# Kernel optimization log

Measured on AMD Instinct MI355X. Metric: run time of the kernel, lower is better.

## Reference

```python
import jax, jax.numpy as jnp
import numpy as np

NUM_BINS_X = 128; NUM_BINS_Y = 128
XL, XH, YL, YH = 0.0, 1000.0, 0.0, 1000.0
NUM_NETS = 100000
NUM_NODES = 200000
NUM_MOVABLE = 180000
NUM_PINS = 400000
UNIT_H_CAP = 1.5
UNIT_V_CAP = 1.4
MAX_RATE = 2.0
MIN_RATE = 1.0 / MAX_RATE
BIN_SX = (XH - XL) / NUM_BINS_X
BIN_SY = (YH - YL) / NUM_BINS_Y


def setup_inputs() -> dict:
    key = jax.random.key(0)
    k1, k2, k3, k4, k5, k6, k7, k8 = jax.random.split(key, 8)
    pos = jnp.concatenate([
        jax.random.uniform(k1, (NUM_NODES,), jnp.float32, XL, XH - 8.0),
        jax.random.uniform(k2, (NUM_NODES,), jnp.float32, YL, YH - 8.0)])
    pin_pos = jnp.concatenate([
        jax.random.uniform(k3, (NUM_PINS,), jnp.float32, XL, XH),
        jax.random.uniform(k4, (NUM_PINS,), jnp.float32, YL, YH)])
    node_size_x = jax.random.uniform(k5, (NUM_NODES,), jnp.float32, 1.0, 8.0)
    node_size_y = jax.random.uniform(k6, (NUM_NODES,), jnp.float32, 1.0, 8.0)
    # 4 pins per net (uniform ragged layout); flat_netpin is a permutation of pins
    netpin_start = jnp.arange(NUM_NETS + 1, dtype=jnp.int32) * (NUM_PINS // NUM_NETS)
    flat_netpin = jax.random.permutation(k7, NUM_PINS).astype(jnp.int32)
    net_weights = jax.random.uniform(k8, (NUM_NETS,), jnp.float32, 0.5, 1.5)
    return dict(pos=pos, pin_pos=pin_pos, node_size_x=node_size_x,
                node_size_y=node_size_y, net_weights=net_weights,
                netpin_start=netpin_start, flat_netpin=flat_netpin)


def _bin_edges(lo, size, n):
    l = lo + jnp.arange(n, dtype=jnp.float32) * size
    return l, l + size


def _overlap(lo_e, hi_e, lo, hi):
    # per-interval overlap of [lo, hi] with each bin [lo_e, hi_e]; >=0
    return jnp.clip(jnp.minimum(hi_e[None, :], hi[:, None]) -
                    jnp.maximum(lo_e[None, :], lo[:, None]), 0.0, None)


def reference(pos, pin_pos, node_size_x, node_size_y, net_weights,
              netpin_start, flat_netpin):
    # ---- phase 1: per-net bbox (ragged gather) + RUDY demand binning ----
    lengths = netpin_start[1:] - netpin_start[:-1]                      # [N]
    net_ids = jnp.repeat(jnp.arange(NUM_NETS, dtype=jnp.int32), lengths,
                         total_repeat_length=NUM_PINS)                  # [P]
    px = pin_pos[flat_netpin]
    py = pin_pos[flat_netpin + NUM_PINS]
    x_min = jax.ops.segment_min(px, net_ids, num_segments=NUM_NETS)
    x_max = jax.ops.segment_max(px, net_ids, num_segments=NUM_NETS)
    y_min = jax.ops.segment_min(py, net_ids, num_segments=NUM_NETS)
    y_max = jax.ops.segment_max(py, net_ids, num_segments=NUM_NETS)

    bxl, bxr = _bin_edges(XL, BIN_SX, NUM_BINS_X)
    byl, byr = _bin_edges(YL, BIN_SY, NUM_BINS_Y)
    ox = _overlap(bxl, bxr, x_min, x_max)                               # [N, BX]
    oy = _overlap(byl, byr, y_min, y_max)                               # [N, BY]
    dx = x_max - x_min
    dy = y_max - y_min
    # horizontal demand per bin = wt * overlap / (y_max - y_min); vertical analog
    cx = jnp.where(dy > 0, net_weights / jnp.where(dy > 0, dy, 1.0), 0.0)
    cy = jnp.where(dx > 0, net_weights / jnp.where(dx > 0, dx, 1.0), 0.0)
    map_x = jnp.einsum('nx,ny->xy', ox * cx[:, None], oy)               # [BX, BY]
    map_y = jnp.einsum('nx,ny->xy', ox * cy[:, None], oy)

    bin_area = BIN_SX * BIN_SY
    ux = map_x / (bin_area * UNIT_H_CAP)
    uy = map_y / (bin_area * UNIT_V_CAP)
    util = jnp.clip(jnp.maximum(ux, uy), MIN_RATE, MAX_RATE)            # [BX, BY]

    # ---- phase 2: per movable node, overlap-weighted utilization read-back ----
    nx = pos[:NUM_MOVABLE]
    ny = pos[NUM_NODES:NUM_NODES + NUM_MOVABLE]
    sx = node_size_x[:NUM_MOVABLE]
    sy = node_size_y[:NUM_MOVABLE]
    oxn = _overlap(bxl, bxr, nx, nx + sx)                               # [M, BX]
    oyn = _overlap(byl, byr, ny, ny + sy)                               # [M, BY]
    tmp = jnp.einsum('mx,xy->my', oxn, util)                            # [M, BY]
    instance_route_area = jnp.sum(tmp * oyn, axis=1)                    # [M]
    return instance_route_area
```

## Files before the change

### kernel.cpp

```cpp
#include <hip/hip_runtime.h>

constexpr int   NB         = 128;
constexpr int   NCELL      = NB * NB;
constexpr int   NFL        = 2 * NCELL;
constexpr float S          = 7.8125f;
constexpr int   NUM_NETS   = 100000;
constexpr int   NUM_NODES  = 200000;
constexpr int   NUM_MOVABLE= 180000;
constexpr int   NUM_PINS   = 400000;
constexpr float UNIT_H_CAP = 1.5f;
constexpr float UNIT_V_CAP = 1.4f;

#define TPB    1024
#define NDB    256
#define NCHUNK 8

__device__ __forceinline__ float edgef(int t) { return (float)t * S; }

__device__ __forceinline__ int bin_of(float v) {
    int t = (int)floorf(v / S);
    while (edgef(t + 1) <= v) ++t;
    while (edgef(t)     >  v) --t;
    return t;
}

__device__ __forceinline__ float phi(int t, float lo, float hi) {
    return fminf(fmaxf(edgef(t), lo), hi);
}

__global__ __launch_bounds__(TPB) void net_diff_kernel(
    const float* __restrict__ pin_pos,
    const float* __restrict__ net_weights,
    const int*   __restrict__ nps,
    const int*   __restrict__ fnp,
    float* __restrict__ P) {
    extern __shared__ float Dl[];
    const int tid = threadIdx.x;

    float4* D4 = (float4*)Dl;
    for (int i = tid; i < NFL / 4; i += TPB) D4[i] = make_float4(0, 0, 0, 0);
    __syncthreads();

    const int per = (NUM_NETS + gridDim.x - 1) / gridDim.x;
    const int n0  = blockIdx.x * per;
    const int n1  = min(n0 + per, NUM_NETS);
    const int l   = tid & 3;
    const int g   = tid >> 2;
    constexpr int GP = TPB / 4;

    for (int n = n0 + g; n < n1; n += GP) {
        int s = nps[n], e = nps[n + 1];
        bool ok = (e > s);
        float xmin, xmax, ymin, ymax;
        if (ok && (e - s == 4)) {
            int pin = fnp[s + l];
            float xv = pin_pos[pin];
            float yv = pin_pos[pin + NUM_PINS];
            xmin = xv; xmax = xv; ymin = yv; ymax = yv;
        } else {
            xmin = 1e30f; xmax = -1e30f; ymin = 1e30f; ymax = -1e30f;
            if (ok && l == 0) {
                for (int p = s; p < e; ++p) {
                    int pin = fnp[p];
                    float px = pin_pos[pin];
                    float py = pin_pos[pin + NUM_PINS];
                    xmin = fminf(xmin, px); xmax = fmaxf(xmax, px);
                    ymin = fminf(ymin, py); ymax = fmaxf(ymax, py);
                }
            }
        }
        xmin = fminf(xmin, __shfl_xor(xmin, 1));
        xmin = fminf(xmin, __shfl_xor(xmin, 2));
        xmax = fmaxf(xmax, __shfl_xor(xmax, 1));
        xmax = fmaxf(xmax, __shfl_xor(xmax, 2));
        ymin = fminf(ymin, __shfl_xor(ymin, 1));
        ymin = fminf(ymin, __shfl_xor(ymin, 2));
        ymax = fmaxf(ymax, __shfl_xor(ymax, 1));
        ymax = fmaxf(ymax, __shfl_xor(ymax, 2));
        if (!ok) continue;

        float w  = net_weights[n];
        float dx = xmax - xmin, dy = ymax - ymin;
        float cx = (dy > 0.f) ? w / dy : 0.f;
        float cy = (dx > 0.f) ? w / dx : 0.f;
        if (cx == 0.f && cy == 0.f) continue;

        int ax = bin_of(xmin), bx = bin_of(xmax);
        int row; bool has;
        if      (l == 0) { row = ax;     has = true; }
        else if (l == 1) { row = ax + 1; has = true; }
        else if (l == 2) { row = bx;     has = (bx > ax + 1); }
        else             { row = bx + 1; has = (bx > ax); }
        if (!has || row >= NB) continue;
        float fi = phi(row + 1, xmin, xmax) - 2.f * phi(row, xmin, xmax)
                 + phi(row - 1, xmin, xmax);
        if (fi == 0.f) continue;

        int ay = bin_of(ymin), by = bin_of(ymax);
        #pragma unroll
        for (int j = 0; j < 4; ++j) {
            int col; bool hj;
            if      (j == 0) { col = ay;     hj = true; }
            else if (j == 1) { col = ay + 1; hj = true; }
            else if (j == 2) { col = by;     hj = (by > ay + 1); }
            else             { col = by + 1; hj = (by > ay); }
            if (!hj || col >= NB) continue;
            float fj = phi(col + 1, ymin, ymax) - 2.f * phi(col, ymin, ymax)
                     + phi(col - 1, ymin, ymax);
            float t = fi * fj;
            if (t == 0.f) continue;
            int cell = row * NB + col;
            if (cx != 0.f) atomicAdd(&Dl[cell],         cx * t);
            if (cy != 0.f) atomicAdd(&Dl[NCELL + cell], cy * t);
        }
    }
    __syncthreads();

    float4* Pb = (float4*)(P + (size_t)blockIdx.x * NFL);
    for (int i = tid; i < NFL / 4; i += TPB) Pb[i] = D4[i];
}

__global__ __launch_bounds__(256) void reduce_kernel(
    const float4* __restrict__ P,
    float4* __restrict__ Rc,
    int B) {
    constexpr int NF4 = NFL / 4;
    int g = blockIdx.y * blockDim.x + threadIdx.x;
    int chunk = blockIdx.x;
    float4 a0 = {0,0,0,0}, a1 = {0,0,0,0}, a2 = {0,0,0,0}, a3 = {0,0,0,0};
    int b = chunk;
    for (; b + 3 * NCHUNK < B; b += 4 * NCHUNK) {
        float4 v0 = P[(size_t)(b             ) * NF4 + g];
        float4 v1 = P[(size_t)(b +     NCHUNK) * NF4 + g];
        float4 v2 = P[(size_t)(b + 2 * NCHUNK) * NF4 + g];
        float4 v3 = P[(size_t)(b + 3 * NCHUNK) * NF4 + g];
        a0.x += v0.x; a0.y += v0.y; a0.z += v0.z; a0.w += v0.w;
        a1.x += v1.x; a1.y += v1.y; a1.z += v1.z; a1.w += v1.w;
        a2.x += v2.x; a2.y += v2.y; a2.z += v2.z; a2.w += v2.w;
        a3.x += v3.x; a3.y += v3.y; a3.z += v3.z; a3.w += v3.w;
    }
    for (; b < B; b += NCHUNK) {
        float4 v = P[(size_t)b * NF4 + g];
        a0.x += v.x; a0.y += v.y; a0.z += v.z; a0.w += v.w;
    }
    float4 r;
    r.x = (a0.x + a1.x) + (a2.x + a3.x);
    r.y = (a0.y + a1.y) + (a2.y + a3.y);
    r.z = (a0.z + a1.z) + (a2.z + a3.z);
    r.w = (a0.w + a1.w) + (a2.w + a3.w);
    Rc[(size_t)chunk * NF4 + g] = r;
}

__global__ __launch_bounds__(NB) void scan_x_kernel(
    const float* __restrict__ Rc,
    float2* __restrict__ Xp) {
    __shared__ float2 sm[NB];
    int col = blockIdx.x;
    int t = threadIdx.x;
    int idx = t * NB + col;
    float2 v = make_float2(0.f, 0.f);
    #pragma unroll
    for (int c = 0; c < NCHUNK; ++c) {
        v.x += Rc[(size_t)c * NFL + idx];
        v.y += Rc[(size_t)c * NFL + NCELL + idx];
    }
    sm[t] = v;
    __syncthreads();
    #pragma unroll
    for (int off = 1; off < NB; off <<= 1) {
        float2 cur = sm[t];
        float2 add = (t >= off) ? sm[t - off] : make_float2(0.f, 0.f);
        __syncthreads();
        cur.x += add.x; cur.y += add.y;
        sm[t] = cur;
        __syncthreads();
    }
    Xp[idx] = sm[t];
}

__global__ __launch_bounds__(NB) void scan_y_kernel(
    const float2* __restrict__ Xp,
    float* __restrict__ util) {
    __shared__ float2 sm[NB];
    int row = blockIdx.x;
    int t = threadIdx.x;
    sm[t] = Xp[row * NB + t];
    __syncthreads();
    #pragma unroll
    for (int off = 1; off < NB; off <<= 1) {
        float2 cur = sm[t];
        float2 add = (t >= off) ? sm[t - off] : make_float2(0.f, 0.f);
        __syncthreads();
        cur.x += add.x; cur.y += add.y;
        sm[t] = cur;
        __syncthreads();
    }
    constexpr float invx = 1.f / (S * S * UNIT_H_CAP);
    constexpr float invy = 1.f / (S * S * UNIT_V_CAP);
    float2 r = sm[t];
    float u = fmaxf(r.x * invx, r.y * invy);
    util[row * NB + t] = fminf(fmaxf(u, 0.5f), 2.0f);
}

__global__ __launch_bounds__(256) void node_kernel(
    const float* __restrict__ pos,
    const float* __restrict__ nsx,
    const float* __restrict__ nsy,
    const float* __restrict__ util,
    float* __restrict__ out) {
    int m = blockIdx.x * blockDim.x + threadIdx.x;
    if (m >= NUM_MOVABLE) return;
    float x  = pos[m];
    float y  = pos[NUM_NODES + m];
    float xh = x + nsx[m];
    float yh = y + nsy[m];
    int ax = max(0,      (int)floorf(x  / S) - 1);
    int bx = min(NB - 1, (int)floorf(xh / S) + 1);
    int ay = max(0,      (int)floorf(y  / S) - 1);
    int by = min(NB - 1, (int)floorf(yh / S) + 1);
    float acc = 0.f;
    for (int i = ax; i <= bx; ++i) {
        float ov = fminf(edgef(i + 1), xh) - fmaxf(edgef(i), x);
        if (ov <= 0.f) continue;
        float inner = 0.f;
        for (int j = ay; j <= by; ++j) {
            float ovy = fminf(edgef(j + 1), yh) - fmaxf(edgef(j), y);
            if (ovy > 0.f) inner += ovy * util[i * NB + j];
        }
        acc += ov * inner;
    }
    out[m] = acc;
}

extern "C" void kernel_launch(void* const* d_in, const int* in_sizes, int n_in,
                              void* d_out, int out_size, void* d_ws, size_t ws_size,
                              hipStream_t stream) {
    const float* pos      = (const float*)d_in[0];
    const float* pin_pos  = (const float*)d_in[1];
    const float* nsx      = (const float*)d_in[2];
    const float* nsy      = (const float*)d_in[3];
    const float* nw       = (const float*)d_in[4];
    const int*   npstart  = (const int*)d_in[5];
    const int*   fnp      = (const int*)d_in[6];
    float*       out      = (float*)d_out;

    float* w    = (float*)d_ws;
    float* Rc   = w;                           w += NCHUNK * NFL;
    float* Xp   = w;                           w += NFL;
    float* util = w;                           w += NCELL;
    float* P    = w;

    size_t fixed = (size_t)(w - (float*)d_ws) * sizeof(float);
    int B = NDB;
    if (ws_size > fixed) {
        size_t fit = (ws_size - fixed) / ((size_t)NFL * sizeof(float));
        if ((size_t)B > fit) B = (int)fit;
    } else {
        B = 1;
    }
    if (B < 1) B = 1;

    (void)hipFuncSetAttribute((const void*)net_diff_kernel,
                              hipFuncAttributeMaxDynamicSharedMemorySize,
                              NFL * (int)sizeof(float));

    net_diff_kernel<<<B, TPB, NFL * sizeof(float), stream>>>(
        pin_pos, nw, npstart, fnp, P);
    {
        dim3 g(NCHUNK, NFL / 4 / 256);
        reduce_kernel<<<g, 256, 0, stream>>>(
            (const float4*)P, (float4*)Rc, B);
    }
    scan_x_kernel<<<NB, NB, 0, stream>>>(Rc, (float2*)Xp);
    scan_y_kernel<<<NB, NB, 0, stream>>>((const float2*)Xp, util);
    node_kernel<<<(NUM_MOVABLE + 255) / 256, 256, 0, stream>>>(
        pos, nsx, nsy, util, out);
}
```

Measured before the change: 115.0 us.

## Split RUDY maps across block pairs and fuse the two prefix scans

Each net-binning block now accumulates only one demand map, horizontal or vertical, chosen by block parity. This halves the per-block LDS histogram and halves the partial-map traffic written to and read back from global memory. The cost is that every net's bounding box is gathered and computed twice, once per map type. The separate x and y scan kernels are replaced by one single-block kernel that runs serial column and row scans in padded LDS. That removes a launch and the intermediate buffer, but leaves only 128 threads doing the serial work.

Measured after the change: 124.6 us. 1.08x slower.

```diff
diff --git a/kernel.cpp b/kernel.cpp
--- a/kernel.cpp
+++ b/kernel.cpp
@@ -2,7 +2,6 @@
 
 constexpr int   NB         = 128;
 constexpr int   NCELL      = NB * NB;
-constexpr int   NFL        = 2 * NCELL;
 constexpr float S          = 7.8125f;
 constexpr int   NUM_NETS   = 100000;
 constexpr int   NUM_NODES  = 200000;
@@ -13,7 +12,9 @@
 
 #define TPB    1024
 #define NDB    256
+#define NET_LDS_BYTES (96*1024)
 #define NCHUNK 8
+#define PAD    129
 
 __device__ __forceinline__ float edgef(int t) { return (float)t * S; }
 
@@ -38,11 +39,14 @@
     const int tid = threadIdx.x;
 
     float4* D4 = (float4*)Dl;
-    for (int i = tid; i < NFL / 4; i += TPB) D4[i] = make_float4(0, 0, 0, 0);
-    __syncthreads();
-
-    const int per = (NUM_NETS + gridDim.x - 1) / gridDim.x;
-    const int n0  = blockIdx.x * per;
+    for (int i = tid; i < NCELL / 4; i += TPB) D4[i] = make_float4(0, 0, 0, 0);
+    __syncthreads();
+
+    const int nchunks = (int)(gridDim.x >> 1);
+    const int chunk   = (int)(blockIdx.x >> 1);
+    const int type    = (int)(blockIdx.x & 1);
+    const int per = (NUM_NETS + nchunks - 1) / nchunks;
+    const int n0  = chunk * per;
     const int n1  = min(n0 + per, NUM_NETS);
     const int l   = tid & 3;
     const int g   = tid >> 2;
@@ -81,9 +85,9 @@
 
         float w  = net_weights[n];
         float dx = xmax - xmin, dy = ymax - ymin;
-        float cx = (dy > 0.f) ? w / dy : 0.f;
-        float cy = (dx > 0.f) ? w / dx : 0.f;
-        if (cx == 0.f && cy == 0.f) continue;
+        float c  = (type == 0) ? ((dy > 0.f) ? w / dy : 0.f)
+                               : ((dx > 0.f) ? w / dx : 0.f);
+        if (c == 0.f) continue;
 
         int ax = bin_of(xmin), bx = bin_of(xmax);
         int row; bool has;
@@ -109,38 +113,36 @@
                      + phi(col - 1, ymin, ymax);
             float t = fi * fj;
             if (t == 0.f) continue;
-            int cell = row * NB + col;
-            if (cx != 0.f) atomicAdd(&Dl[cell],         cx * t);
-            if (cy != 0.f) atomicAdd(&Dl[NCELL + cell], cy * t);
-        }
-    }
-    __syncthreads();
-
-    float4* Pb = (float4*)(P + (size_t)blockIdx.x * NFL);
-    for (int i = tid; i < NFL / 4; i += TPB) Pb[i] = D4[i];
+            atomicAdd(&Dl[row * NB + col], c * t);
+        }
+    }
+    __syncthreads();
+
+    float4* Pb = (float4*)(P + (size_t)blockIdx.x * NCELL);
+    for (int i = tid; i < NCELL / 4; i += TPB) Pb[i] = D4[i];
 }
 
 __global__ __launch_bounds__(256) void reduce_kernel(
     const float4* __restrict__ P,
     float4* __restrict__ Rc,
     int B) {
-    constexpr int NF4 = NFL / 4;
-    int g = blockIdx.y * blockDim.x + threadIdx.x;
+    constexpr int NQ = NCELL / 4;
+    int g = blockIdx.y * 256 + threadIdx.x;
     int chunk = blockIdx.x;
     float4 a0 = {0,0,0,0}, a1 = {0,0,0,0}, a2 = {0,0,0,0}, a3 = {0,0,0,0};
     int b = chunk;
     for (; b + 3 * NCHUNK < B; b += 4 * NCHUNK) {
-        float4 v0 = P[(size_t)(b             ) * NF4 + g];
-        float4 v1 = P[(size_t)(b +     NCHUNK) * NF4 + g];
-        float4 v2 = P[(size_t)(b + 2 * NCHUNK) * NF4 + g];
-        float4 v3 = P[(size_t)(b + 3 * NCHUNK) * NF4 + g];
+        float4 v0 = P[(size_t)(b             ) * NQ + g];
+        float4 v1 = P[(size_t)(b +     NCHUNK) * NQ + g];
+        float4 v2 = P[(size_t)(b + 2 * NCHUNK) * NQ + g];
+        float4 v3 = P[(size_t)(b + 3 * NCHUNK) * NQ + g];
         a0.x += v0.x; a0.y += v0.y; a0.z += v0.z; a0.w += v0.w;
         a1.x += v1.x; a1.y += v1.y; a1.z += v1.z; a1.w += v1.w;
         a2.x += v2.x; a2.y += v2.y; a2.z += v2.z; a2.w += v2.w;
         a3.x += v3.x; a3.y += v3.y; a3.z += v3.z; a3.w += v3.w;
     }
     for (; b < B; b += NCHUNK) {
-        float4 v = P[(size_t)b * NF4 + g];
+        float4 v = P[(size_t)b * NQ + g];
         a0.x += v.x; a0.y += v.y; a0.z += v.z; a0.w += v.w;
     }
     float4 r;
@@ -148,58 +150,48 @@
     r.y = (a0.y + a1.y) + (a2.y + a3.y);
     r.z = (a0.z + a1.z) + (a2.z + a3.z);
     r.w = (a0.w + a1.w) + (a2.w + a3.w);
-    Rc[(size_t)chunk * NF4 + g] = r;
-}
-
-__global__ __launch_bounds__(NB) void scan_x_kernel(
+    Rc[(size_t)chunk * NQ + g] = r;
+}
+
+__global__ __launch_bounds__(1024) void scanxy_kernel(
     const float* __restrict__ Rc,
-    float2* __restrict__ Xp) {
-    __shared__ float2 sm[NB];
-    int col = blockIdx.x;
-    int t = threadIdx.x;
-    int idx = t * NB + col;
-    float2 v = make_float2(0.f, 0.f);
-    #pragma unroll
-    for (int c = 0; c < NCHUNK; ++c) {
-        v.x += Rc[(size_t)c * NFL + idx];
-        v.y += Rc[(size_t)c * NFL + NCELL + idx];
-    }
-    sm[t] = v;
-    __syncthreads();
-    #pragma unroll
-    for (int off = 1; off < NB; off <<= 1) {
-        float2 cur = sm[t];
-        float2 add = (t >= off) ? sm[t - off] : make_float2(0.f, 0.f);
-        __syncthreads();
-        cur.x += add.x; cur.y += add.y;
-        sm[t] = cur;
-        __syncthreads();
-    }
-    Xp[idx] = sm[t];
-}
-
-__global__ __launch_bounds__(NB) void scan_y_kernel(
-    const float2* __restrict__ Xp,
     float* __restrict__ util) {
-    __shared__ float2 sm[NB];
-    int row = blockIdx.x;
-    int t = threadIdx.x;
-    sm[t] = Xp[row * NB + t];
-    __syncthreads();
-    #pragma unroll
-    for (int off = 1; off < NB; off <<= 1) {
-        float2 cur = sm[t];
-        float2 add = (t >= off) ? sm[t - off] : make_float2(0.f, 0.f);
-        __syncthreads();
-        cur.x += add.x; cur.y += add.y;
-        sm[t] = cur;
-        __syncthreads();
-    }
-    constexpr float invx = 1.f / (S * S * UNIT_H_CAP);
-    constexpr float invy = 1.f / (S * S * UNIT_V_CAP);
-    float2 r = sm[t];
-    float u = fmaxf(r.x * invx, r.y * invy);
-    util[row * NB + t] = fminf(fmaxf(u, 0.5f), 2.0f);
+    extern __shared__ float2 M[];
+    int tid = threadIdx.x;
+    for (int cell = tid; cell < NCELL; cell += 1024) {
+        int r = cell >> 7, c = cell & (NB - 1);
+        float vx = Rc[0 * NCELL + cell] + Rc[2 * NCELL + cell]
+                 + Rc[4 * NCELL + cell] + Rc[6 * NCELL + cell];
+        float vy = Rc[1 * NCELL + cell] + Rc[3 * NCELL + cell]
+                 + Rc[5 * NCELL + cell] + Rc[7 * NCELL + cell];
+        M[r * PAD + c] = make_float2(vx, vy);
+    }
+    __syncthreads();
+    if (tid < NB) {
+        int col = tid;
+        float2 acc = M[col];
+        for (int r = 1; r < NB; ++r) {
+            float2 v = M[r * PAD + col];
+            acc.x += v.x; acc.y += v.y;
+            M[r * PAD + col] = acc;
+        }
+    }
+    __syncthreads();
+    if (tid < NB) {
+        int row = tid;
+        constexpr float invx = 1.f / (S * S * UNIT_H_CAP);
+        constexpr float invy = 1.f / (S * S * UNIT_V_CAP);
+        float2 acc = make_float2(0.f, 0.f);
+        for (int c = 0; c < NB; ++c) {
+            float2 v = M[row * PAD + c];
+            acc.x += v.x; acc.y += v.y;
+            float u = fmaxf(acc.x * invx, acc.y * invy);
+            M[row * PAD + c].x = fminf(fmaxf(u, 0.5f), 2.0f);
+        }
+    }
+    __syncthreads();
+    for (int cell = tid; cell < NCELL; cell += 1024)
+        util[cell] = M[(cell >> 7) * PAD + (cell & (NB - 1))].x;
 }
 
 __global__ __launch_bounds__(256) void node_kernel(
@@ -245,34 +237,37 @@
     float*       out      = (float*)d_out;
 
     float* w    = (float*)d_ws;
-    float* Rc   = w;                           w += NCHUNK * NFL;
-    float* Xp   = w;                           w += NFL;
+    float* Rc   = w;                           w += NCHUNK * NCELL;
     float* util = w;                           w += NCELL;
     float* P    = w;
 
     size_t fixed = (size_t)(w - (float*)d_ws) * sizeof(float);
     int B = NDB;
     if (ws_size > fixed) {
-        size_t fit = (ws_size - fixed) / ((size_t)NFL * sizeof(float));
+        size_t fit = (ws_size - fixed) / ((size_t)NCELL * sizeof(float));
         if ((size_t)B > fit) B = (int)fit;
     } else {
-        B = 1;
-    }
-    if (B < 1) B = 1;
+        B = 2;
+    }
+    B &= ~1;
+    if (B < 2) B = 2;
 
     (void)hipFuncSetAttribute((const void*)net_diff_kernel,
                               hipFuncAttributeMaxDynamicSharedMemorySize,
-                              NFL * (int)sizeof(float));
-
-    net_diff_kernel<<<B, TPB, NFL * sizeof(float), stream>>>(
+                              NET_LDS_BYTES);
+    (void)hipFuncSetAttribute((const void*)scanxy_kernel,
+                              hipFuncAttributeMaxDynamicSharedMemorySize,
+                              NB * PAD * (int)sizeof(float2));
+
+    net_diff_kernel<<<B, TPB, NET_LDS_BYTES, stream>>>(
         pin_pos, nw, npstart, fnp, P);
     {
-        dim3 g(NCHUNK, NFL / 4 / 256);
+        dim3 g(NCHUNK, NCELL / 4 / 256);
         reduce_kernel<<<g, 256, 0, stream>>>(
             (const float4*)P, (float4*)Rc, B);
     }
-    scan_x_kernel<<<NB, NB, 0, stream>>>(Rc, (float2*)Xp);
-    scan_y_kernel<<<NB, NB, 0, stream>>>((const float2*)Xp, util);
+    scanxy_kernel<<<1, 1024, NB * PAD * (int)sizeof(float2), stream>>>(
+        Rc, util);
     node_kernel<<<(NUM_MOVABLE + 255) / 256, 256, 0, stream>>>(
         pos, nsx, nsy, util, out);
 }
```

## Fuse 2D prefix scans into one LDS kernel and process two nets per iteration

Applied to the files above, without the earlier changes.

Replaces the separate column and row scan kernels, and the global intermediate buffer between them, with a single 1024-thread block. That block does both prefix passes in padded LDS using segmented scans. Separately, the net binning loop now handles two nets per iteration, issuing both nets' gathers before either scatter so memory latency overlaps. The single-block scan cuts a launch and a global round trip, but runs on one CU with 16-step serial segments. The two-net loop raises register pressure.

New measurement: 126.1 us. 1.1x slower.

```diff
diff --git a/kernel.cpp b/kernel.cpp
--- a/kernel.cpp
+++ b/kernel.cpp
@@ -15,6 +15,10 @@
 #define NDB    256
 #define NCHUNK 8
 
+#define PADM2  129
+#define SEG    8
+#define SEGR   16
+
 __device__ __forceinline__ float edgef(int t) { return (float)t * S; }
 
 __device__ __forceinline__ int bin_of(float v) {
@@ -26,6 +30,56 @@
 
 __device__ __forceinline__ float phi(int t, float lo, float hi) {
     return fminf(fmaxf(edgef(t), lo), hi);
+}
+
+__device__ __forceinline__ void grp_reduce(float& xmin, float& xmax,
+                                           float& ymin, float& ymax) {
+    xmin = fminf(xmin, __shfl_xor(xmin, 1));
+    xmin = fminf(xmin, __shfl_xor(xmin, 2));
+    xmax = fmaxf(xmax, __shfl_xor(xmax, 1));
+    xmax = fmaxf(xmax, __shfl_xor(xmax, 2));
+    ymin = fminf(ymin, __shfl_xor(ymin, 1));
+    ymin = fminf(ymin, __shfl_xor(ymin, 2));
+    ymax = fmaxf(ymax, __shfl_xor(ymax, 1));
+    ymax = fmaxf(ymax, __shfl_xor(ymax, 2));
+}
+
+__device__ __forceinline__ void scatter_net(
+    float xmin, float xmax, float ymin, float ymax, float w,
+    int l, float* __restrict__ Dl) {
+    float dx = xmax - xmin, dy = ymax - ymin;
+    float cx = (dy > 0.f) ? w / dy : 0.f;
+    float cy = (dx > 0.f) ? w / dx : 0.f;
+    if (cx == 0.f && cy == 0.f) return;
+
+    int ax = bin_of(xmin), bx = bin_of(xmax);
+    int row; bool has;
+    if      (l == 0) { row = ax;     has = true; }
+    else if (l == 1) { row = ax + 1; has = true; }
+    else if (l == 2) { row = bx;     has = (bx > ax + 1); }
+    else             { row = bx + 1; has = (bx > ax); }
+    if (!has || row >= NB) return;
+    float fi = phi(row + 1, xmin, xmax) - 2.f * phi(row, xmin, xmax)
+             + phi(row - 1, xmin, xmax);
+    if (fi == 0.f) return;
+
+    int ay = bin_of(ymin), by = bin_of(ymax);
+    #pragma unroll
+    for (int j = 0; j < 4; ++j) {
+        int col; bool hj;
+        if      (j == 0) { col = ay;     hj = true; }
+        else if (j == 1) { col = ay + 1; hj = true; }
+        else if (j == 2) { col = by;     hj = (by > ay + 1); }
+        else             { col = by + 1; hj = (by > ay); }
+        if (!hj || col >= NB) continue;
+        float fj = phi(col + 1, ymin, ymax) - 2.f * phi(col, ymin, ymax)
+                 + phi(col - 1, ymin, ymax);
+        float t = fi * fj;
+        if (t == 0.f) continue;
+        int cell = row * NB + col;
+        if (cx != 0.f) atomicAdd(&Dl[cell],         cx * t);
+        if (cy != 0.f) atomicAdd(&Dl[NCELL + cell], cy * t);
+    }
 }
 
 __global__ __launch_bounds__(TPB) void net_diff_kernel(
@@ -48,70 +102,59 @@
     const int g   = tid >> 2;
     constexpr int GP = TPB / 4;
 
-    for (int n = n0 + g; n < n1; n += GP) {
-        int s = nps[n], e = nps[n + 1];
-        bool ok = (e > s);
-        float xmin, xmax, ymin, ymax;
-        if (ok && (e - s == 4)) {
-            int pin = fnp[s + l];
-            float xv = pin_pos[pin];
-            float yv = pin_pos[pin + NUM_PINS];
-            xmin = xv; xmax = xv; ymin = yv; ymax = yv;
-        } else {
-            xmin = 1e30f; xmax = -1e30f; ymin = 1e30f; ymax = -1e30f;
-            if (ok && l == 0) {
-                for (int p = s; p < e; ++p) {
-                    int pin = fnp[p];
-                    float px = pin_pos[pin];
-                    float py = pin_pos[pin + NUM_PINS];
-                    xmin = fminf(xmin, px); xmax = fmaxf(xmax, px);
-                    ymin = fminf(ymin, py); ymax = fmaxf(ymax, py);
+    for (int nA = n0 + g; nA < n1; nA += 2 * GP) {
+        const int nB = nA + GP;
+        const bool hasB = (nB < n1);
+
+        int sA = nps[nA], eA = nps[nA + 1];
+        int sB = 0, eB = 0;
+        if (hasB) { sB = nps[nB]; eB = nps[nB + 1]; }
+        const bool okA = (eA > sA), okB = hasB && (eB > sB);
+        const bool fA = okA && (eA - sA == 4);
+        const bool fB = okB && (eB - sB == 4);
+        int pinA = fA ? fnp[sA + l] : 0;
+        int pinB = fB ? fnp[sB + l] : 0;
+        float xvA = 0.f, yvA = 0.f, xvB = 0.f, yvB = 0.f;
+        if (fA) { xvA = pin_pos[pinA]; yvA = pin_pos[pinA + NUM_PINS]; }
+        if (fB) { xvB = pin_pos[pinB]; yvB = pin_pos[pinB + NUM_PINS]; }
+        float wA = okA ? net_weights[nA] : 0.f;
+        float wB = okB ? net_weights[nB] : 0.f;
+
+        {
+            float xmin, xmax, ymin, ymax;
+            if (fA) { xmin = xvA; xmax = xvA; ymin = yvA; ymax = yvA; }
+            else {
+                xmin = 1e30f; xmax = -1e30f; ymin = 1e30f; ymax = -1e30f;
+                if (okA && l == 0) {
+                    for (int p = sA; p < eA; ++p) {
+                        int pin = fnp[p];
+                        float px = pin_pos[pin];
+                        float py = pin_pos[pin + NUM_PINS];
+                        xmin = fminf(xmin, px); xmax = fmaxf(xmax, px);
+                        ymin = fminf(ymin, py); ymax = fmaxf(ymax, py);
+                    }
                 }
             }
-        }
-        xmin = fminf(xmin, __shfl_xor(xmin, 1));
-        xmin = fminf(xmin, __shfl_xor(xmin, 2));
-        xmax = fmaxf(xmax, __shfl_xor(xmax, 1));
-        xmax = fmaxf(xmax, __shfl_xor(xmax, 2));
-        ymin = fminf(ymin, __shfl_xor(ymin, 1));
-        ymin = fminf(ymin, __shfl_xor(ymin, 2));
-        ymax = fmaxf(ymax, __shfl_xor(ymax, 1));
-        ymax = fmaxf(ymax, __shfl_xor(ymax, 2));
-        if (!ok) continue;
-
-        float w  = net_weights[n];
-        float dx = xmax - xmin, dy = ymax - ymin;
-        float cx = (dy > 0.f) ? w / dy : 0.f;
-        float cy = (dx > 0.f) ? w / dx : 0.f;
-        if (cx == 0.f && cy == 0.f) continue;
-
-        int ax = bin_of(xmin), bx = bin_of(xmax);
-        int row; bool has;
-        if      (l == 0) { row = ax;     has = true; }
-        else if (l == 1) { row = ax + 1; has = true; }
-        else if (l == 2) { row = bx;     has = (bx > ax + 1); }
-        else             { row = bx + 1; has = (bx > ax); }
-        if (!has || row >= NB) continue;
-        float fi = phi(row + 1, xmin, xmax) - 2.f * phi(row, xmin, xmax)
-                 + phi(row - 1, xmin, xmax);
-        if (fi == 0.f) continue;
-
-        int ay = bin_of(ymin), by = bin_of(ymax);
-        #pragma unroll
-        for (int j = 0; j < 4; ++j) {
-            int col; bool hj;
-            if      (j == 0) { col = ay;     hj = true; }
-            else if (j == 1) { col = ay + 1; hj = true; }
-            else if (j == 2) { col = by;     hj = (by > ay + 1); }
-            else             { col = by + 1; hj = (by > ay); }
-            if (!hj || col >= NB) continue;
-            float fj = phi(col + 1, ymin, ymax) - 2.f * phi(col, ymin, ymax)
-                     + phi(col - 1, ymin, ymax);
-            float t = fi * fj;
-            if (t == 0.f) continue;
-            int cell = row * NB + col;
-            if (cx != 0.f) atomicAdd(&Dl[cell],         cx * t);
-            if (cy != 0.f) atomicAdd(&Dl[NCELL + cell], cy * t);
+            grp_reduce(xmin, xmax, ymin, ymax);
+            if (okA) scatter_net(xmin, xmax, ymin, ymax, wA, l, Dl);
+        }
+        {
+            float xmin, xmax, ymin, ymax;
+            if (fB) { xmin = xvB; xmax = xvB; ymin = yvB; ymax = yvB; }
+            else {
+                xmin = 1e30f; xmax = -1e30f; ymin = 1e30f; ymax = -1e30f;
+                if (okB && l == 0) {
+                    for (int p = sB; p < eB; ++p) {
+                        int pin = fnp[p];
+                        float px = pin_pos[pin];
+                        float py = pin_pos[pin + NUM_PINS];
+                        xmin = fminf(xmin, px); xmax = fmaxf(xmax, px);
+                        ymin = fminf(ymin, py); ymax = fmaxf(ymax, py);
+                    }
+                }
+            }
+            grp_reduce(xmin, xmax, ymin, ymax);
+            if (okB) scatter_net(xmin, xmax, ymin, ymax, wB, l, Dl);
         }
     }
     __syncthreads();
@@ -151,55 +194,88 @@
     Rc[(size_t)chunk * NF4 + g] = r;
 }
 
-__global__ __launch_bounds__(NB) void scan_x_kernel(
+__global__ __launch_bounds__(1024) void scanxy_kernel(
     const float* __restrict__ Rc,
-    float2* __restrict__ Xp) {
-    __shared__ float2 sm[NB];
-    int col = blockIdx.x;
-    int t = threadIdx.x;
-    int idx = t * NB + col;
-    float2 v = make_float2(0.f, 0.f);
-    #pragma unroll
-    for (int c = 0; c < NCHUNK; ++c) {
-        v.x += Rc[(size_t)c * NFL + idx];
-        v.y += Rc[(size_t)c * NFL + NCELL + idx];
-    }
-    sm[t] = v;
+    float* __restrict__ util) {
+    extern __shared__ float2 M[];
+    float2* T = M + NB * PADM2;
+    const int tid = threadIdx.x;
+
+    {
+        const int c = tid & (NB - 1);
+        const int s = tid >> 7;
+        float2 run = make_float2(0.f, 0.f);
+        for (int i = 0; i < SEGR; ++i) {
+            int r = s * SEGR + i;
+            int idx = r * NB + c;
+            float vx = 0.f, vy = 0.f;
+            #pragma unroll
+            for (int ch = 0; ch < NCHUNK; ++ch) {
+                vx += Rc[(size_t)ch * NFL + idx];
+                vy += Rc[(size_t)ch * NFL + NCELL + idx];
+            }
+            run.x += vx; run.y += vy;
+            M[r * PADM2 + c] = run;
+        }
+        T[s * NB + c] = run;
+        __syncthreads();
+        float2 v = T[s * NB + c];
+        #pragma unroll
+        for (int off = 1; off < SEG; off <<= 1) {
+            float2 add = make_float2(0.f, 0.f);
+            if (s >= off) add = T[(s - off) * NB + c];
+            __syncthreads();
+            v.x += add.x; v.y += add.y;
+            T[s * NB + c] = v;
+            __syncthreads();
+        }
+        float2 e = make_float2(0.f, 0.f);
+        if (s > 0) e = T[(s - 1) * NB + c];
+        for (int i = 0; i < SEGR; ++i) {
+            int r = s * SEGR + i;
+            float2 m = M[r * PADM2 + c];
+            m.x += e.x; m.y += e.y;
+            M[r * PADM2 + c] = m;
+        }
+    }
     __syncthreads();
-    #pragma unroll
-    for (int off = 1; off < NB; off <<= 1) {
-        float2 cur = sm[t];
-        float2 add = (t >= off) ? sm[t - off] : make_float2(0.f, 0.f);
+
+    {
+        const int r = tid & (NB - 1);
+        const int s = tid >> 7;
+        float2 run = make_float2(0.f, 0.f);
+        for (int i = 0; i < SEGR; ++i) {
+            int c = s * SEGR + i;
+            float2 v = M[r * PADM2 + c];
+            run.x += v.x; run.y += v.y;
+            M[r * PADM2 + c] = run;
+        }
+        T[s * NB + r] = run;
         __syncthreads();
-        cur.x += add.x; cur.y += add.y;
-        sm[t] = cur;
-        __syncthreads();
-    }
-    Xp[idx] = sm[t];
-}
-
-__global__ __launch_bounds__(NB) void scan_y_kernel(
-    const float2* __restrict__ Xp,
-    float* __restrict__ util) {
-    __shared__ float2 sm[NB];
-    int row = blockIdx.x;
-    int t = threadIdx.x;
-    sm[t] = Xp[row * NB + t];
+        float2 v = T[s * NB + r];
+        #pragma unroll
+        for (int off = 1; off < SEG; off <<= 1) {
+            float2 add = make_float2(0.f, 0.f);
+            if (s >= off) add = T[(s - off) * NB + r];
+            __syncthreads();
+            v.x += add.x; v.y += add.y;
+            T[s * NB + r] = v;
+            __syncthreads();
+        }
+        float2 e = make_float2(0.f, 0.f);
+        if (s > 0) e = T[(s - 1) * NB + r];
+        constexpr float invx = 1.f / (S * S * UNIT_H_CAP);
+        constexpr float invy = 1.f / (S * S * UNIT_V_CAP);
+        for (int i = 0; i < SEGR; ++i) {
+            int c = s * SEGR + i;
+            float2 m = M[r * PADM2 + c];
+            float u = fmaxf((m.x + e.x) * invx, (m.y + e.y) * invy);
+            M[r * PADM2 + c].x = fminf(fmaxf(u, 0.5f), 2.0f);
+        }
+    }
     __syncthreads();
-    #pragma unroll
-    for (int off = 1; off < NB; off <<= 1) {
-        float2 cur = sm[t];
-        float2 add = (t >= off) ? sm[t - off] : make_float2(0.f, 0.f);
-        __syncthreads();
-        cur.x += add.x; cur.y += add.y;
-        sm[t] = cur;
-        __syncthreads();
-    }
-    constexpr float invx = 1.f / (S * S * UNIT_H_CAP);
-    constexpr float invy = 1.f / (S * S * UNIT_V_CAP);
-    float2 r = sm[t];
-    float u = fmaxf(r.x * invx, r.y * invy);
-    util[row * NB + t] = fminf(fmaxf(u, 0.5f), 2.0f);
+    for (int cell = tid; cell < NCELL; cell += 1024)
+        util[cell] = M[(cell >> 7) * PADM2 + (cell & (NB - 1))].x;
 }
 
 __global__ __launch_bounds__(256) void node_kernel(
@@ -246,7 +322,6 @@
 
     float* w    = (float*)d_ws;
     float* Rc   = w;                           w += NCHUNK * NFL;
-    float* Xp   = w;                           w += NFL;
     float* util = w;                           w += NCELL;
     float* P    = w;
 
@@ -260,9 +335,14 @@
     }
     if (B < 1) B = 1;
 
+    const int scan_lds = (NB * PADM2 + SEG * NB) * (int)sizeof(float2);
+
     (void)hipFuncSetAttribute((const void*)net_diff_kernel,
                               hipFuncAttributeMaxDynamicSharedMemorySize,
                               NFL * (int)sizeof(float));
+    (void)hipFuncSetAttribute((const void*)scanxy_kernel,
+                              hipFuncAttributeMaxDynamicSharedMemorySize,
+                              scan_lds);
 
     net_diff_kernel<<<B, TPB, NFL * sizeof(float), stream>>>(
         pin_pos, nw, npstart, fnp, P);
@@ -271,8 +351,7 @@
         reduce_kernel<<<g, 256, 0, stream>>>(
             (const float4*)P, (float4*)Rc, B);
     }
-    scan_x_kernel<<<NB, NB, 0, stream>>>(Rc, (float2*)Xp);
-    scan_y_kernel<<<NB, NB, 0, stream>>>((const float2*)Xp, util);
+    scanxy_kernel<<<1, 1024, scan_lds, stream>>>(Rc, util);
     node_kernel<<<(NUM_MOVABLE + 255) / 256, 256, 0, stream>>>(
         pos, nsx, nsy, util, out);
 }
```
